# Performance work log

Hardware: AMD Instinct MI355X
Metric: run time of the kernel (lower is better)

The kernel has to match this reference:

```python
import jax, jax.numpy as jnp
import numpy as np

B, T, C, NH = 2, 2048, 1024, 16
D = C // NH


def _ln(t, eps=1e-6):
    m = jnp.mean(t, axis=-1, keepdims=True)
    v = jnp.mean((t - m) ** 2, axis=-1, keepdims=True)
    return (t - m) * jax.lax.rsqrt(v + eps)


def _rot(t):
    # pairwise rotation: (q0,q1,q2,q3,...) -> (-q1,q0,-q3,q2,...)
    t2 = t.reshape(*t.shape[:-1], -1, 2)
    r = jnp.stack([-t2[..., 1], t2[..., 0]], axis=-1)
    return r.reshape(t.shape)


def setup_inputs() -> dict:
    key = jax.random.key(0)
    ks = jax.random.split(key, 8)
    x = jax.random.normal(ks[0], (B, T, C), jnp.float32)
    c = jax.random.normal(ks[1], (B, 1, C), jnp.float32)
    # RoPE-style angles for pe[0]=cos, pe[1]=sin; pe[2] is a positive per-position scale
    pos = jnp.arange(T, dtype=jnp.float32)
    inv = 1.0 / (10000.0 ** (jnp.arange(0, D, 2, dtype=jnp.float32) / D))
    th = jnp.repeat(pos[:, None] * inv[None, :], 2, axis=-1)  # (T, D)
    pe_cos = jnp.cos(th)[None, None]
    pe_sin = jnp.sin(th)[None, None]
    pe_scale = jnp.exp(0.01 * jax.random.normal(ks[2], (1, 1, T, D), jnp.float32))
    # causal mask: True = masked
    cm = jnp.arange(T)[None, :] > jnp.arange(T)[:, None]
    mask = jnp.broadcast_to(cm[None, None], (1, B, T, T))
    s = 0.02
    qkv_w = s * jax.random.normal(ks[3], (3 * C, C), jnp.float32)
    qkv_b = jnp.zeros((3 * C,), jnp.float32)
    w1 = s * jax.random.normal(ks[4], (4 * C, C), jnp.float32)
    b1 = jnp.zeros((4 * C,), jnp.float32)
    w2 = s * jax.random.normal(ks[5], (C, 4 * C), jnp.float32)
    b2 = jnp.zeros((C,), jnp.float32)
    ada_w = s * jax.random.normal(ks[6], (6 * C, C), jnp.float32)
    ada_b = 0.1 * jax.random.normal(ks[7], (6 * C,), jnp.float32)
    return dict(x=x, pe_cos=pe_cos, pe_sin=pe_sin, pe_scale=pe_scale, c=c, mask=mask,
                qkv_w=qkv_w, qkv_b=qkv_b, w1=w1, b1=b1, w2=w2, b2=b2,
                ada_w=ada_w, ada_b=ada_b)


def reference(x, pe_cos, pe_sin, pe_scale, c, mask, qkv_w, qkv_b, w1, b1, w2, b2, ada_w, ada_b):
    b, t, ch = x.shape
    nh = NH
    d = ch // nh
    tp = (2 * d) ** 0.5
    # AdaLN modulation
    cm = jax.nn.selu(c) @ ada_w.T + ada_b            # (b,1,6c)
    shift, scale, gate, shift_f, scale_f, gate_f = jnp.split(cm, 6, axis=-1)
    # attention branch
    h = _ln(x) * (1 + scale) + shift
    qkv = h @ qkv_w.T + qkv_b                        # (b,t,3c)
    q, k, v = jnp.split(qkv, 3, axis=-1)
    heads = lambda a: a.reshape(b, t, nh, d).transpose(0, 2, 1, 3)  # (b,nh,t,d)
    q, k, v = heads(q), heads(k), heads(v)
    q = (q * pe_cos + _rot(q) * pe_sin) * pe_scale
    k = (k * pe_cos + _rot(k) * pe_sin) / pe_scale
    scores = jnp.einsum('bhqd,bhkd->bhqk', q, k) / tp
    scores = jnp.where(mask[0][:, None], -jnp.inf, scores)  # mask (b,1,t,t) broadcast over heads
    alpha = jax.nn.softmax(scores, axis=-1)
    attn = jnp.einsum('bhqk,bhkd->bhqd', alpha, v).transpose(0, 2, 1, 3).reshape(b, t, ch)
    x = x + gate * attn
    # gated FFN branch (dropout is eval-mode identity)
    h2 = _ln(x) * (1 + scale_f) + shift_f
    ff = jax.nn.selu(h2 @ w1.T + b1) @ w2.T + b2
    return x + gate_f * ff
```

## Files before the change

kernel.cpp:

```cpp
#include <hip/hip_runtime.h>

#define Bn 2
#define Tn 2048
#define Cn 1024
#define NHn 16

typedef __attribute__((ext_vector_type(8))) short s16x8;
typedef __attribute__((ext_vector_type(4))) short s16x4;
typedef __attribute__((ext_vector_type(4))) float f32x4;
typedef __attribute__((ext_vector_type(8))) unsigned short u16x8;
typedef __attribute__((ext_vector_type(4))) unsigned short u16x4;
typedef const __attribute__((address_space(1))) void* gas_t;
typedef __attribute__((address_space(3))) void* las_t;

__device__ __forceinline__ void gl_lds16(const void* g, void* l) {
  __builtin_amdgcn_global_load_lds((gas_t)g, (las_t)l, 16, 0, 0);
}

__device__ __forceinline__ float bf2f(unsigned short u) {
  unsigned int x = ((unsigned int)u) << 16;
  float f; __builtin_memcpy(&f, &x, 4); return f;
}
__device__ __forceinline__ unsigned short f2bf(float f) {
  unsigned int x; __builtin_memcpy(&x, &f, 4);
  x += 0x7fffu + ((x >> 16) & 1u);
  return (unsigned short)(x >> 16);
}
__device__ __forceinline__ unsigned int cvt_pk_bf16(float a, float b) {
  unsigned int r;
  asm("v_cvt_pk_bf16_f32 %0, %1, %2" : "=v"(r) : "v"(a), "v"(b));
  return r;
}
__device__ __forceinline__ f32x4 mfma16_bf16(s16x4 a, s16x4 b, f32x4 c) {
#if defined(__has_builtin)
#if __has_builtin(__builtin_amdgcn_mfma_f32_16x16x16bf16_1k)
  return __builtin_amdgcn_mfma_f32_16x16x16bf16_1k(a, b, c, 0, 0, 0);
#else
  return c;
#endif
#else
  return c;
#endif
}
__device__ __forceinline__ float selu_f(float x) {
  const float SC = 1.0507009873554805f, AL = 1.6732632423543772f;
  return x > 0.f ? SC * x : SC * AL * (__expf(x) - 1.f);
}
__device__ __forceinline__ float waveRS(float v) {
#pragma unroll
  for (int m = 32; m; m >>= 1) v += __shfl_xor(v, m, 64);
  return v;
}

template <int BK>
__device__ __forceinline__ int swz_stage(int row, int sl) {
  if constexpr (BK == 32) return sl ^ ((row >> 1) & 3);
  else return sl ^ (row & 7);
}
template <int BK>
__device__ __forceinline__ int swz_read(int rr, int kk, int lg) {
  if constexpr (BK == 32) return lg ^ ((rr >> 1) & 3);
  else return (kk * 4 + lg) ^ (rr & 7);
}

__global__ __launch_bounds__(256) void prep_kernel(
    const float* __restrict__ qkv_w, const float* __restrict__ w1,
    const float* __restrict__ w2, unsigned short* __restrict__ qkvw_bf,
    unsigned short* __restrict__ w1_bf, unsigned short* __restrict__ w2_bf,
    const float* __restrict__ cin, const float* __restrict__ ada_w,
    const float* __restrict__ ada_b, float* __restrict__ cm) {
  const int blk = blockIdx.x;
  const int tid = threadIdx.x;
  if (blk < 11264) {
    const float* in; unsigned short* out; size_t base;
    if (blk < 3072)      { in = qkv_w; out = qkvw_bf; base = (size_t)blk * 1024; }
    else if (blk < 7168) { in = w1;    out = w1_bf;   base = (size_t)(blk - 3072) * 1024; }
    else                 { in = w2;    out = w2_bf;   base = (size_t)(blk - 7168) * 1024; }
    size_t i = base + (size_t)tid * 4;
    float4 v = *(const float4*)(in + i);
    u16x4 o;
    o.x = f2bf(v.x); o.y = f2bf(v.y); o.z = f2bf(v.z); o.w = f2bf(v.w);
    *(u16x4*)(out + i) = o;
  } else {
    const int w = tid >> 6, l = tid & 63;
    const int j = (blk - 11264) * 4 + w;
    __shared__ float sc[2][1024];
#pragma unroll
    for (int i = 0; i < 4; ++i) {
      int idx = i * 256 + tid;
      sc[0][idx] = selu_f(cin[idx]);
      sc[1][idx] = selu_f(cin[1024 + idx]);
    }
    __syncthreads();
    const float* wr_ = ada_w + (size_t)j * 1024;
    float a0 = 0.f, a1 = 0.f;
#pragma unroll
    for (int i = 0; i < 4; ++i) {
      float4 wv = *(const float4*)(wr_ + (i * 64 + l) * 4);
      const float* s0 = sc[0] + (i * 64 + l) * 4;
      const float* s1 = sc[1] + (i * 64 + l) * 4;
      a0 += wv.x * s0[0] + wv.y * s0[1] + wv.z * s0[2] + wv.w * s0[3];
      a1 += wv.x * s1[0] + wv.y * s1[1] + wv.z * s1[2] + wv.w * s1[3];
    }
    a0 = waveRS(a0);
    a1 = waveRS(a1);
    if (l == 0) {
      const float bb = ada_b[j];
      cm[j] = a0 + bb;
      cm[6144 + j] = a1 + bb;
    }
  }
}

__global__ __launch_bounds__(256) void ln_mod(
    const float* __restrict__ xin, const float* __restrict__ cm,
    unsigned short* __restrict__ hout, int shift_off, int scale_off) {
  const int tid = threadIdx.x;
  const int row = blockIdx.x;
  const int b = row >> 11;
  const float* xr = xin + (size_t)row * 1024;
  float v[4]; float s = 0.f, s2 = 0.f;
#pragma unroll
  for (int i = 0; i < 4; ++i) {
    v[i] = xr[i * 256 + tid]; s += v[i]; s2 += v[i] * v[i];
  }
  __shared__ float rs[8];
  s = waveRS(s); s2 = waveRS(s2);
  const int w = tid >> 6, l = tid & 63;
  if (l == 0) { rs[w] = s; rs[4 + w] = s2; }
  __syncthreads();
  s = rs[0] + rs[1] + rs[2] + rs[3];
  s2 = rs[4] + rs[5] + rs[6] + rs[7];
  float mean = s * (1.f / 1024.f);
  float var = s2 * (1.f / 1024.f) - mean * mean;
  float rstd = rsqrtf(var + 1e-6f);
  const float* cb = cm + b * 6144;
#pragma unroll
  for (int i = 0; i < 4; ++i) {
    int ch = i * 256 + tid;
    float hv = (v[i] - mean) * rstd * (1.f + cb[scale_off + ch]) + cb[shift_off + ch];
    hout[(size_t)row * 1024 + ch] = f2bf(hv);
  }
}

template <int MODE, int TM, int BK>
__global__ __launch_bounds__(256) void gemm_bt(
    const unsigned short* __restrict__ A, const unsigned short* __restrict__ Bw,
    const float* __restrict__ bias, unsigned short* __restrict__ obf,
    float* __restrict__ of32, const float* __restrict__ resid,
    const float* __restrict__ cm, int M, int N, int K) {
  constexpr int MR = TM / 32;
  constexpr int CPR = BK / 8;
  constexpr int ACH = TM * BK / 2048;
  constexpr int BCH = 128 * BK / 2048;
  constexpr int KK = BK / 32;
  constexpr int LPI = ACH + BCH;
  __shared__ unsigned short As[2 * TM * BK];
  __shared__ unsigned short Bs[2 * 128 * BK];
  const int tid = threadIdx.x;
  const int gx = gridDim.x;
  int flat = blockIdx.y * gx + blockIdx.x;
  const int cpx = (gx * gridDim.y) >> 3;
  flat = (flat & 7) * cpx + (flat >> 3);
  const int bm = flat / gx, bn = flat % gx;
  const int w = tid >> 6, l = tid & 63;
  const int wr = w >> 1, wc = w & 1;
  const int lr = l & 15, lg = l >> 4;

  f32x4 acc[MR][4];
#pragma unroll
  for (int m = 0; m < MR; ++m)
#pragma unroll
    for (int n = 0; n < 4; ++n) acc[m][n] = (f32x4){0.f, 0.f, 0.f, 0.f};

  const size_t abase = (size_t)bm * TM * K;
  const size_t bbase = (size_t)bn * 128 * K;

#define GEMM_STAGE(KT, HALF)                                                        \
  do {                                                                              \
    const int ko_ = (KT) * BK;                                                      \
    const int hf_ = (HALF);                                                         \
    _Pragma("unroll")                                                               \
    for (int j = 0; j < ACH; ++j) {                                                 \
      const int c = tid + j * 256;                                                  \
      const int row_ = c / CPR, sl_ = c % CPR;                                      \
      const int kcg = swz_stage<BK>(row_, sl_);                                     \
      gl_lds16(A + abase + (size_t)row_ * K + kcg * 8 + ko_,                        \
               As + hf_ * TM * BK + c * 8);                                         \
    }                                                                               \
    _Pragma("unroll")                                                               \
    for (int j = 0; j < BCH; ++j) {                                                 \
      const int c = tid + j * 256;                                                  \
      const int row_ = c / CPR, sl_ = c % CPR;                                      \
      const int kcg = swz_stage<BK>(row_, sl_);                                     \
      gl_lds16(Bw + bbase + (size_t)row_ * K + kcg * 8 + ko_,                       \
               Bs + hf_ * 128 * BK + c * 8);                                        \
    }                                                                               \
  } while (0)

  const int nkt = K / BK;
  GEMM_STAGE(0, 0);
  for (int kt = 0; kt < nkt; ++kt) {
    const int cur = kt & 1;
    if (kt + 1 < nkt) {
      GEMM_STAGE(kt + 1, cur ^ 1);
      asm volatile("s_waitcnt vmcnt(%0)" ::"n"(LPI) : "memory");
    } else {
      asm volatile("s_waitcnt vmcnt(0)" ::: "memory");
    }
    __builtin_amdgcn_sched_barrier(0);
    __builtin_amdgcn_s_barrier();
    __builtin_amdgcn_sched_barrier(0);
    s16x8 af[MR][KK], bf[4][KK];
#pragma unroll
    for (int m = 0; m < MR; ++m) {
      const int rr = wr * (TM / 2) + m * 16 + lr;
#pragma unroll
      for (int kk = 0; kk < KK; ++kk) {
        const int kc = swz_read<BK>(rr, kk, lg);
        af[m][kk] = *(const s16x8*)(As + cur * TM * BK + rr * BK + kc * 8);
      }
    }
#pragma unroll
    for (int n = 0; n < 4; ++n) {
      const int rr = wc * 64 + n * 16 + lr;
#pragma unroll
      for (int kk = 0; kk < KK; ++kk) {
        const int kc = swz_read<BK>(rr, kk, lg);
        bf[n][kk] = *(const s16x8*)(Bs + cur * 128 * BK + rr * BK + kc * 8);
      }
    }
#pragma unroll
    for (int kk = 0; kk < KK; ++kk)
#pragma unroll
      for (int m = 0; m < MR; ++m)
#pragma unroll
        for (int n = 0; n < 4; ++n)
          acc[m][n] = __builtin_amdgcn_mfma_f32_16x16x32_bf16(af[m][kk], bf[n][kk], acc[m][n], 0, 0, 0);
    asm volatile("" ::: "memory");
    __builtin_amdgcn_s_barrier();
    __builtin_amdgcn_sched_barrier(0);
  }
#undef GEMM_STAGE

#pragma unroll
  for (int m = 0; m < MR; ++m) {
#pragma unroll
    for (int n = 0; n < 4; ++n) {
      const int col = bn * 128 + wc * 64 + n * 16 + lr;
      const float bv = bias[col];
#pragma unroll
      for (int r = 0; r < 4; ++r) {
        const int row = bm * TM + wr * (TM / 2) + m * 16 + lg * 4 + r;
        float v = acc[m][n][r] + bv;
        if (MODE == 0) {
          obf[(size_t)row * N + col] = f2bf(v);
        } else if (MODE == 1) {
          obf[(size_t)row * N + col] = f2bf(selu_f(v));
        } else {
          const int b = row >> 11;
          const float g = cm[b * 6144 + 5 * 1024 + col];
          of32[(size_t)row * N + col] = resid[(size_t)row * N + col] + g * v;
        }
      }
    }
  }
}

__global__ __launch_bounds__(256) void rope_pack(
    const unsigned short* __restrict__ qkv, const float* __restrict__ cosp,
    const float* __restrict__ sinp, const float* __restrict__ scalep,
    unsigned short* __restrict__ Qo, unsigned short* __restrict__ Ko,
    unsigned short* __restrict__ Vt) {
  const int tid = threadIdx.x;
  const int blk = blockIdx.x;
  const int tt = blk & 31, bh = blk >> 5;
  const int b = bh >> 4, h = bh & 15;
  const int t0 = tt * 64;
  __shared__ __align__(16) unsigned short tile[64][192];
#pragma unroll
  for (int i = 0; i < 6; ++i) {
    int cidx = i * 256 + tid;
    int r = cidx / 24, sg = cidx % 24;
    int colbase = (sg < 8) ? (h * 64 + sg * 8)
                : (sg < 16) ? (Cn + h * 64 + (sg - 8) * 8)
                            : (2 * Cn + h * 64 + (sg - 16) * 8);
    u16x8 v = *(const u16x8*)(qkv + (size_t)(b * Tn + t0 + r) * 3072 + colbase);
    *(u16x8*)(&tile[r][sg * 8]) = v;
  }
  __syncthreads();
  {
    const int t = tid >> 2, d0 = (tid & 3) * 16;
    const int tg = t0 + t;
    float co[16], si[16], sc[16];
#pragma unroll
    for (int i = 0; i < 4; ++i) {
      *(float4*)(co + i * 4) = *(const float4*)(cosp + (size_t)tg * 64 + d0 + i * 4);
      *(float4*)(si + i * 4) = *(const float4*)(sinp + (size_t)tg * 64 + d0 + i * 4);
      *(float4*)(sc + i * 4) = *(const float4*)(scalep + (size_t)tg * 64 + d0 + i * 4);
    }
    u16x8 qv[2], kv[2];
    unsigned short* qo = (unsigned short*)qv;
    unsigned short* ko = (unsigned short*)kv;
#pragma unroll
    for (int i = 0; i < 8; ++i) {
      int d = 2 * i;
      float q0 = bf2f(tile[t][d0 + d]), q1 = bf2f(tile[t][d0 + d + 1]);
      float k0 = bf2f(tile[t][64 + d0 + d]), k1 = bf2f(tile[t][64 + d0 + d + 1]);
      float qr0 = (q0 * co[d] - q1 * si[d]) * sc[d];
      float qr1 = (q1 * co[d + 1] + q0 * si[d + 1]) * sc[d + 1];
      float kr0 = (k0 * co[d] - k1 * si[d]) / sc[d];
      float kr1 = (k1 * co[d + 1] + k0 * si[d + 1]) / sc[d + 1];
      qo[d] = f2bf(qr0); qo[d + 1] = f2bf(qr1);
      ko[d] = f2bf(kr0); ko[d + 1] = f2bf(kr1);
    }
    size_t obase = ((size_t)bh * Tn + tg) * 64 + d0;
    *(u16x8*)(Qo + obase) = qv[0];
    *(u16x8*)(Qo + obase + 8) = qv[1];
    *(u16x8*)(Ko + obase) = kv[0];
    *(u16x8*)(Ko + obase + 8) = kv[1];
  }
  {
    const int d = tid >> 2, ksub = tid & 3;
    const int kt16 = (t0 >> 4) + ksub;
    u16x8 vv[2];
    unsigned short* vp = (unsigned short*)vv;
#pragma unroll
    for (int j = 0; j < 16; ++j) vp[j] = tile[ksub * 16 + j][128 + d];
    size_t obase = (((size_t)bh * 128 + kt16) * 4 + (d >> 4)) * 256 + (d & 15) * 16;
    *(u16x8*)(Vt + obase) = vv[0];
    *(u16x8*)(Vt + obase + 8) = vv[1];
  }
}

#define ATTN_LOAD(KB, KF, VF)                                                          \
  do {                                                                                 \
    const int kb_ = (KB);                                                              \
    _Pragma("unroll")                                                                  \
    for (int cc = 0; cc < 2; ++cc) {                                                   \
      const unsigned short* Kp = Kbase + (size_t)(kb_ + cc * 16 + lr) * 64 + lg * 8;   \
      KF[cc][0] = *(const s16x8*)(Kp);                                                 \
      KF[cc][1] = *(const s16x8*)(Kp + 32);                                            \
    }                                                                                  \
    _Pragma("unroll")                                                                  \
    for (int dt = 0; dt < 4; ++dt)                                                     \
      _Pragma("unroll")                                                                \
      for (int cc = 0; cc < 2; ++cc)                                                   \
        VF[dt][cc] = *(const s16x4*)(Vbase + (size_t)(((kb_ >> 4) + cc) * 4 + dt) *    \
                                     256 + lr * 16 + lg * 4);                          \
  } while (0)

#define ATTN_COMP(KB, KF, VF, DOMASK)                                                  \
  do {                                                                                 \
    const int kb_ = (KB);                                                              \
    const bool dm_ = (DOMASK);                                                         \
    f32x4 st[2][2];                                                                    \
    _Pragma("unroll")                                                                  \
    for (int qt = 0; qt < 2; ++qt)                                                     \
      _Pragma("unroll")                                                                \
      for (int cc = 0; cc < 2; ++cc) {                                                 \
        f32x4 t = (f32x4){0.f, 0.f, 0.f, 0.f};                                         \
        t = __builtin_amdgcn_mfma_f32_16x16x32_bf16(KF[cc][0], qa[qt][0], t, 0, 0, 0); \
        t = __builtin_amdgcn_mfma_f32_16x16x32_bf16(KF[cc][1], qa[qt][1], t, 0, 0, 0); \
        st[qt][cc] = t;                                                                \
      }                                                                                \
    _Pragma("unroll")                                                                  \
    for (int qt = 0; qt < 2; ++qt) {                                                   \
      const int q = q0w + qt * 16 + lr;                                                \
      float tmax = -1e30f;                                                             \
      _Pragma("unroll")                                                                \
      for (int cc = 0; cc < 2; ++cc)                                                   \
        _Pragma("unroll")                                                              \
        for (int r = 0; r < 4; ++r) {                                                  \
          float s = st[qt][cc][r] * inv_tp;                                            \
          if (dm_) {                                                                   \
            const int key = kb_ + cc * 16 + lg * 4 + r;                                \
            if (key > q) s = -1e30f;                                                   \
          }                                                                            \
          st[qt][cc][r] = s;                                                           \
          tmax = fmaxf(tmax, s);                                                       \
        }                                                                              \
      tmax = fmaxf(tmax, __shfl_xor(tmax, 16, 64));                                    \
      tmax = fmaxf(tmax, __shfl_xor(tmax, 32, 64));                                    \
      if (__any(tmax > mrow[qt] + 8.f)) {                                              \
        const float mn = fmaxf(mrow[qt], tmax);                                        \
        const float alpha = __expf(mrow[qt] - mn);                                     \
        mrow[qt] = mn;                                                                 \
        lsum[qt] *= alpha;                                                             \
        _Pragma("unroll")                                                              \
        for (int dt = 0; dt < 4; ++dt)                                                 \
          _Pragma("unroll")                                                            \
          for (int r = 0; r < 4; ++r) o[qt][dt][r] *= alpha;                           \
      }                                                                                \
      float p[2][4];                                                                   \
      float part = 0.f;                                                                \
      _Pragma("unroll")                                                                \
      for (int cc = 0; cc < 2; ++cc)                                                   \
        _Pragma("unroll")                                                              \
        for (int r = 0; r < 4; ++r) {                                                  \
          p[cc][r] = __expf(st[qt][cc][r] - mrow[qt]);                                 \
          part += p[cc][r];                                                            \
        }                                                                              \
      part += __shfl_xor(part, 16, 64);                                                \
      part += __shfl_xor(part, 32, 64);                                                \
      lsum[qt] += part;                                                                \
      s16x4 pb[2];                                                                     \
      _Pragma("unroll")                                                                \
      for (int cc = 0; cc < 2; ++cc) {                                                 \
        union { unsigned int u[2]; s16x4 v; } pk;                                      \
        pk.u[0] = cvt_pk_bf16(p[cc][0], p[cc][1]);                                     \
        pk.u[1] = cvt_pk_bf16(p[cc][2], p[cc][3]);                                     \
        pb[cc] = pk.v;                                                                 \
      }                                                                                \
      _Pragma("unroll")                                                                \
      for (int dt = 0; dt < 4; ++dt)                                                   \
        _Pragma("unroll")                                                              \
        for (int cc = 0; cc < 2; ++cc)                                                 \
          o[qt][dt] = mfma16_bf16(VF[dt][cc], pb[cc], o[qt][dt]);                      \
    }                                                                                  \
  } while (0)

__global__ __launch_bounds__(256) void attn_kernel(
    const unsigned short* __restrict__ Q, const unsigned short* __restrict__ Kb,
    const unsigned short* __restrict__ Vt, const float* __restrict__ x,
    const float* __restrict__ cm, float* __restrict__ x2) {
  const int blk = blockIdx.x;
  const int xcd = blk & 7, idx = blk >> 3;
  const int bh = xcd + 8 * (idx & 3);
  const int s_ = idx >> 2;
  const int qchunk = (s_ < 8) ? (15 - s_) : (s_ - 8);
  const int b = bh >> 4, h = bh & 15;
  const int tid = threadIdx.x;
  const int w = tid >> 6, l = tid & 63;
  const int lr = l & 15, lg = l >> 4;
  const int q0w = qchunk * 128 + w * 32;
  const float inv_tp = 0.08838834764831845f;

  const unsigned short* Kbase = Kb + (size_t)bh * Tn * 64;
  const unsigned short* Vbase = Vt + (size_t)bh * Tn * 64;

  const unsigned short* Qp = Q + ((size_t)bh * Tn + q0w) * 64;
  s16x8 qa[2][2];
#pragma unroll
  for (int qt = 0; qt < 2; ++qt) {
    qa[qt][0] = *(const s16x8*)(Qp + (qt * 16 + lr) * 64 + lg * 8);
    qa[qt][1] = *(const s16x8*)(Qp + (qt * 16 + lr) * 64 + 32 + lg * 8);
  }

  f32x4 o[2][4];
#pragma unroll
  for (int qt = 0; qt < 2; ++qt)
#pragma unroll
    for (int dt = 0; dt < 4; ++dt) o[qt][dt] = (f32x4){0.f, 0.f, 0.f, 0.f};
  float mrow[2] = {-1e30f, -1e30f}, lsum[2] = {0.f, 0.f};

  const int N = (q0w >> 5) + 1;
  s16x8 kf0[2][2], kf1[2][2];
  s16x4 vf0[4][2], vf1[4][2];

  ATTN_LOAD(0, kf0, vf0);
  int kt = 0;
  for (; kt + 2 <= N; kt += 2) {
    ATTN_LOAD((kt + 1) * 32, kf1, vf1);
    ATTN_COMP(kt * 32, kf0, vf0, false);
    if (kt + 2 < N) ATTN_LOAD((kt + 2) * 32, kf0, vf0);
    ATTN_COMP((kt + 1) * 32, kf1, vf1, kt + 1 == N - 1);
  }
  if (kt < N) ATTN_COMP(kt * 32, kf0, vf0, true);

#pragma unroll
  for (int qt = 0; qt < 2; ++qt) {
    const float rinv = 1.f / lsum[qt];
    const int q = q0w + qt * 16 + lr;
#pragma unroll
    for (int dt = 0; dt < 4; ++dt) {
      const int colb = h * 64 + dt * 16 + lg * 4;
      const size_t idx2 = ((size_t)b * Tn + q) * Cn + colb;
      float4 xv = *(const float4*)(x + idx2);
      float4 gv = *(const float4*)(cm + b * 6144 + 2048 + colb);
      float4 ov;
      ov.x = xv.x + gv.x * o[qt][dt][0] * rinv;
      ov.y = xv.y + gv.y * o[qt][dt][1] * rinv;
      ov.z = xv.z + gv.z * o[qt][dt][2] * rinv;
      ov.w = xv.w + gv.w * o[qt][dt][3] * rinv;
      *(float4*)(x2 + idx2) = ov;
    }
  }
}

extern "C" void kernel_launch(void* const* d_in, const int* in_sizes, int n_in,
                              void* d_out, int out_size, void* d_ws, size_t ws_size,
                              hipStream_t stream) {
  (void)in_sizes; (void)n_in; (void)out_size; (void)ws_size;
  const float* x = (const float*)d_in[0];
  const float* pe_cos = (const float*)d_in[1];
  const float* pe_sin = (const float*)d_in[2];
  const float* pe_scale = (const float*)d_in[3];
  const float* cc = (const float*)d_in[4];
  const float* qkv_w = (const float*)d_in[6];
  const float* qkv_b = (const float*)d_in[7];
  const float* w1 = (const float*)d_in[8];
  const float* b1 = (const float*)d_in[9];
  const float* w2 = (const float*)d_in[10];
  const float* b2 = (const float*)d_in[11];
  const float* ada_w = (const float*)d_in[12];
  const float* ada_b = (const float*)d_in[13];
  float* out = (float*)d_out;
  char* ws = (char*)d_ws;

  unsigned short* qkvw_bf = (unsigned short*)(ws + 0);
  unsigned short* w1_bf = (unsigned short*)(ws + 6291456);
  unsigned short* w2_bf = (unsigned short*)(ws + 14680064);
  float* cm = (float*)(ws + 23068672);
  unsigned short* h1 = (unsigned short*)(ws + 23117824);
  unsigned short* qkvb = (unsigned short*)(ws + 31506432);
  unsigned short* Qb = (unsigned short*)(ws + 56672256);
  unsigned short* Kb2 = (unsigned short*)(ws + 65060864);
  unsigned short* Vtb = (unsigned short*)(ws + 73449472);
  float* x2b = (float*)(ws + 81838080);
  unsigned short* ff1b = (unsigned short*)(ws + 31506432);

  prep_kernel<<<12800, 256, 0, stream>>>(qkv_w, w1, w2, qkvw_bf, w1_bf, w2_bf,
                                         cc, ada_w, ada_b, cm);
  ln_mod<<<4096, 256, 0, stream>>>(x, cm, h1, 0, 1024);
  gemm_bt<0, 64, 32><<<dim3(24, 64), 256, 0, stream>>>(h1, qkvw_bf, qkv_b, qkvb, nullptr, nullptr, nullptr, 4096, 3072, 1024);
  rope_pack<<<1024, 256, 0, stream>>>(qkvb, pe_cos, pe_sin, pe_scale, Qb, Kb2, Vtb);
  attn_kernel<<<512, 256, 0, stream>>>(Qb, Kb2, Vtb, x, cm, x2b);
  ln_mod<<<4096, 256, 0, stream>>>(x2b, cm, h1, 3072, 4096);
  gemm_bt<1, 128, 64><<<dim3(32, 32), 256, 0, stream>>>(h1, w1_bf, b1, ff1b, nullptr, nullptr, nullptr, 4096, 4096, 1024);
  gemm_bt<2, 64, 64><<<dim3(8, 64), 256, 0, stream>>>(ff1b, w2_bf, b2, nullptr, out, x2b, cm, 4096, 1024, 4096);
}
```

Measured before the change: 257.5 us.

## Fuse RoPE and Q/K/V head packing into the QKV GEMM epilogue

Drops the separate rope_pack kernel. The QKV GEMM epilogue now applies the rotation with a lane shuffle for the pair partner, applies the per-position scale, and writes Q/K in head-major layout and V in the transposed tiled layout directly. This removes a full bf16 round trip of the qkv buffer and one kernel launch. The QKV GEMM tile also changes from 64 to 128 rows, and the epilogue now does scattered 2-byte stores and per-element pe loads.

```diff
diff --git a/kernel.cpp b/kernel.cpp
--- a/kernel.cpp
+++ b/kernel.cpp
@@ -148,7 +148,10 @@
     const unsigned short* __restrict__ A, const unsigned short* __restrict__ Bw,
     const float* __restrict__ bias, unsigned short* __restrict__ obf,
     float* __restrict__ of32, const float* __restrict__ resid,
-    const float* __restrict__ cm, int M, int N, int K) {
+    const float* __restrict__ cm, int M, int N, int K,
+    const float* __restrict__ pe_c, const float* __restrict__ pe_s,
+    const float* __restrict__ pe_sc, unsigned short* __restrict__ q_out,
+    unsigned short* __restrict__ k_out, unsigned short* __restrict__ v_out) {
   constexpr int MR = TM / 32;
   constexpr int CPR = BK / 8;
   constexpr int ACH = TM * BK / 2048;
@@ -249,87 +252,53 @@
     for (int n = 0; n < 4; ++n) {
       const int col = bn * 128 + wc * 64 + n * 16 + lr;
       const float bv = bias[col];
-#pragma unroll
-      for (int r = 0; r < 4; ++r) {
-        const int row = bm * TM + wr * (TM / 2) + m * 16 + lg * 4 + r;
-        float v = acc[m][n][r] + bv;
-        if (MODE == 0) {
-          obf[(size_t)row * N + col] = f2bf(v);
-        } else if (MODE == 1) {
-          obf[(size_t)row * N + col] = f2bf(selu_f(v));
+      if (MODE == 3) {
+        const int row0 = bm * TM + wr * (TM / 2) + m * 16 + lg * 4;
+        const int sec = col >> 10;
+        const int cc2 = col & 1023;
+        const int hh = cc2 >> 6, dd = cc2 & 63;
+        const int bb = row0 >> 11;
+        const int tt0 = row0 & 2047;
+        const int bh = bb * 16 + hh;
+        float vv[4];
+#pragma unroll
+        for (int r = 0; r < 4; ++r) vv[r] = acc[m][n][r] + bv;
+        if (sec < 2) {
+          unsigned short* outp = (sec == 0) ? q_out : k_out;
+#pragma unroll
+          for (int r = 0; r < 4; ++r) {
+            const float pv = __shfl_xor(vv[r], 1, 64);
+            const size_t ti = (size_t)(tt0 + r) * 64 + dd;
+            const float c = pe_c[ti], s = pe_s[ti], sc = pe_sc[ti];
+            float ro = (dd & 1) ? (vv[r] * c + pv * s) : (vv[r] * c - pv * s);
+            ro = (sec == 0) ? ro * sc : ro / sc;
+            outp[((size_t)bh * Tn + tt0 + r) * 64 + dd] = f2bf(ro);
+          }
         } else {
-          const int b = row >> 11;
-          const float g = cm[b * 6144 + 5 * 1024 + col];
-          of32[(size_t)row * N + col] = resid[(size_t)row * N + col] + g * v;
+          u16x4 ov;
+          ov.x = f2bf(vv[0]); ov.y = f2bf(vv[1]);
+          ov.z = f2bf(vv[2]); ov.w = f2bf(vv[3]);
+          const size_t off = (((size_t)bh * 128 + (tt0 >> 4)) * 4 + (dd >> 4)) * 256 +
+                             (size_t)(dd & 15) * 16 + (tt0 & 15);
+          *(u16x4*)(v_out + off) = ov;
+        }
+      } else {
+#pragma unroll
+        for (int r = 0; r < 4; ++r) {
+          const int row = bm * TM + wr * (TM / 2) + m * 16 + lg * 4 + r;
+          float v = acc[m][n][r] + bv;
+          if (MODE == 0) {
+            obf[(size_t)row * N + col] = f2bf(v);
+          } else if (MODE == 1) {
+            obf[(size_t)row * N + col] = f2bf(selu_f(v));
+          } else {
+            const int b = row >> 11;
+            const float g = cm[b * 6144 + 5 * 1024 + col];
+            of32[(size_t)row * N + col] = resid[(size_t)row * N + col] + g * v;
+          }
         }
       }
     }
-  }
-}
-
-__global__ __launch_bounds__(256) void rope_pack(
-    const unsigned short* __restrict__ qkv, const float* __restrict__ cosp,
-    const float* __restrict__ sinp, const float* __restrict__ scalep,
-    unsigned short* __restrict__ Qo, unsigned short* __restrict__ Ko,
-    unsigned short* __restrict__ Vt) {
-  const int tid = threadIdx.x;
-  const int blk = blockIdx.x;
-  const int tt = blk & 31, bh = blk >> 5;
-  const int b = bh >> 4, h = bh & 15;
-  const int t0 = tt * 64;
-  __shared__ __align__(16) unsigned short tile[64][192];
-#pragma unroll
-  for (int i = 0; i < 6; ++i) {
-    int cidx = i * 256 + tid;
-    int r = cidx / 24, sg = cidx % 24;
-    int colbase = (sg < 8) ? (h * 64 + sg * 8)
-                : (sg < 16) ? (Cn + h * 64 + (sg - 8) * 8)
-                            : (2 * Cn + h * 64 + (sg - 16) * 8);
-    u16x8 v = *(const u16x8*)(qkv + (size_t)(b * Tn + t0 + r) * 3072 + colbase);
-    *(u16x8*)(&tile[r][sg * 8]) = v;
-  }
-  __syncthreads();
-  {
-    const int t = tid >> 2, d0 = (tid & 3) * 16;
-    const int tg = t0 + t;
-    float co[16], si[16], sc[16];
-#pragma unroll
-    for (int i = 0; i < 4; ++i) {
-      *(float4*)(co + i * 4) = *(const float4*)(cosp + (size_t)tg * 64 + d0 + i * 4);
-      *(float4*)(si + i * 4) = *(const float4*)(sinp + (size_t)tg * 64 + d0 + i * 4);
-      *(float4*)(sc + i * 4) = *(const float4*)(scalep + (size_t)tg * 64 + d0 + i * 4);
-    }
-    u16x8 qv[2], kv[2];
-    unsigned short* qo = (unsigned short*)qv;
-    unsigned short* ko = (unsigned short*)kv;
-#pragma unroll
-    for (int i = 0; i < 8; ++i) {
-      int d = 2 * i;
-      float q0 = bf2f(tile[t][d0 + d]), q1 = bf2f(tile[t][d0 + d + 1]);
-      float k0 = bf2f(tile[t][64 + d0 + d]), k1 = bf2f(tile[t][64 + d0 + d + 1]);
-      float qr0 = (q0 * co[d] - q1 * si[d]) * sc[d];
-      float qr1 = (q1 * co[d + 1] + q0 * si[d + 1]) * sc[d + 1];
-      float kr0 = (k0 * co[d] - k1 * si[d]) / sc[d];
-      float kr1 = (k1 * co[d + 1] + k0 * si[d + 1]) / sc[d + 1];
-      qo[d] = f2bf(qr0); qo[d + 1] = f2bf(qr1);
-      ko[d] = f2bf(kr0); ko[d + 1] = f2bf(kr1);
-    }
-    size_t obase = ((size_t)bh * Tn + tg) * 64 + d0;
-    *(u16x8*)(Qo + obase) = qv[0];
-    *(u16x8*)(Qo + obase + 8) = qv[1];
-    *(u16x8*)(Ko + obase) = kv[0];
-    *(u16x8*)(Ko + obase + 8) = kv[1];
-  }
-  {
-    const int d = tid >> 2, ksub = tid & 3;
-    const int kt16 = (t0 >> 4) + ksub;
-    u16x8 vv[2];
-    unsigned short* vp = (unsigned short*)vv;
-#pragma unroll
-    for (int j = 0; j < 16; ++j) vp[j] = tile[ksub * 16 + j][128 + d];
-    size_t obase = (((size_t)bh * 128 + kt16) * 4 + (d >> 4)) * 256 + (d & 15) * 16;
-    *(u16x8*)(Vt + obase) = vv[0];
-    *(u16x8*)(Vt + obase + 8) = vv[1];
   }
 }
 
@@ -513,20 +482,24 @@
   unsigned short* w2_bf = (unsigned short*)(ws + 14680064);
   float* cm = (float*)(ws + 23068672);
   unsigned short* h1 = (unsigned short*)(ws + 23117824);
-  unsigned short* qkvb = (unsigned short*)(ws + 31506432);
+  unsigned short* ff1b = (unsigned short*)(ws + 31506432);
   unsigned short* Qb = (unsigned short*)(ws + 56672256);
   unsigned short* Kb2 = (unsigned short*)(ws + 65060864);
   unsigned short* Vtb = (unsigned short*)(ws + 73449472);
   float* x2b = (float*)(ws + 81838080);
-  unsigned short* ff1b = (unsigned short*)(ws + 31506432);
 
   prep_kernel<<<12800, 256, 0, stream>>>(qkv_w, w1, w2, qkvw_bf, w1_bf, w2_bf,
                                          cc, ada_w, ada_b, cm);
   ln_mod<<<4096, 256, 0, stream>>>(x, cm, h1, 0, 1024);
-  gemm_bt<0, 64, 32><<<dim3(24, 64), 256, 0, stream>>>(h1, qkvw_bf, qkv_b, qkvb, nullptr, nullptr, nullptr, 4096, 3072, 1024);
-  rope_pack<<<1024, 256, 0, stream>>>(qkvb, pe_cos, pe_sin, pe_scale, Qb, Kb2, Vtb);
+  gemm_bt<3, 128, 32><<<dim3(24, 32), 256, 0, stream>>>(
+      h1, qkvw_bf, qkv_b, nullptr, nullptr, nullptr, nullptr, 4096, 3072, 1024,
+      pe_cos, pe_sin, pe_scale, Qb, Kb2, Vtb);
   attn_kernel<<<512, 256, 0, stream>>>(Qb, Kb2, Vtb, x, cm, x2b);
   ln_mod<<<4096, 256, 0, stream>>>(x2b, cm, h1, 3072, 4096);
-  gemm_bt<1, 128, 64><<<dim3(32, 32), 256, 0, stream>>>(h1, w1_bf, b1, ff1b, nullptr, nullptr, nullptr, 4096, 4096, 1024);
-  gemm_bt<2, 64, 64><<<dim3(8, 64), 256, 0, stream>>>(ff1b, w2_bf, b2, nullptr, out, x2b, cm, 4096, 1024, 4096);
-}
+  gemm_bt<1, 128, 64><<<dim3(32, 32), 256, 0, stream>>>(
+      h1, w1_bf, b1, ff1b, nullptr, nullptr, nullptr, 4096, 4096, 1024,
+      nullptr, nullptr, nullptr, nullptr, nullptr, nullptr);
+  gemm_bt<2, 64, 64><<<dim3(8, 64), 256, 0, stream>>>(
+      ff1b, w2_bf, b2, nullptr, out, x2b, cm, 4096, 1024, 4096,
+      nullptr, nullptr, nullptr, nullptr, nullptr, nullptr);
+}
```

Result: faster. 239.3 us (-7.1%).
